# Optimization experiments

Hardware: AMD Instinct MI355X
Metric: run time of the kernel (lower is better)

The kernel has to match this reference:

```python
import jax, jax.numpy as jnp
import numpy as np

LATENT_DIM = 512
ASSET_DIM = 8192


def setup_inputs() -> dict:
    key = jax.random.key(0)
    ks = jax.random.split(key, 7)
    d = LATENT_DIM
    s = 1.0 / np.sqrt(d)  # torch Linear default init scale (uniform bound)
    z = jax.random.normal(ks[0], (ASSET_DIM, d), dtype=jnp.float32)
    Wq = jax.random.uniform(ks[1], (d, d), jnp.float32, -s, s)
    Wk = jax.random.uniform(ks[2], (d, d), jnp.float32, -s, s)
    Wv = jax.random.uniform(ks[3], (d, d), jnp.float32, -s, s)
    bq = jax.random.uniform(ks[4], (d,), jnp.float32, -s, s)
    bk = jax.random.uniform(ks[5], (d,), jnp.float32, -s, s)
    bv = jax.random.uniform(ks[6], (d,), jnp.float32, -s, s)
    return {"z": z, "Wq": Wq, "bq": bq, "Wk": Wk, "bk": bk, "Wv": Wv, "bv": bv}


def reference(z, Wq, bq, Wk, bk, Wv, bv):
    # z: (N, D). Single-head self-attention over assets.
    d = z.shape[-1]
    scale = d ** (-0.5)
    q = z @ Wq.T + bq          # (N, D)
    k = z @ Wk.T + bk          # (N, D)
    v = z @ Wv.T + bv          # (N, D)
    scores = jnp.einsum('nd,md->nm', q, k) * scale   # (N, N)
    attn = jax.nn.softmax(scores, axis=-1)
    # Original does attn[:, :, None] * v[None] then sum(dim=1); identical math:
    h = attn @ v               # (N, D)
    return h
```

## Files before the change

kernel.cpp:

```cpp
#include <hip/hip_runtime.h>
#include <hip/hip_bf16.h>
#include <stdint.h>

#define D 512
#define N 8192

typedef __attribute__((ext_vector_type(8))) short short8;
typedef __attribute__((ext_vector_type(4))) float f32x4;

static __device__ __forceinline__ unsigned short f2bf(float f) {
  unsigned int u = __builtin_bit_cast(unsigned int, f);
  u += 0x7fffu + ((u >> 16) & 1u);
  return (unsigned short)(u >> 16);
}
static __device__ __forceinline__ float bf2f(unsigned short s) {
  unsigned int u = ((unsigned int)s) << 16;
  return __builtin_bit_cast(float, u);
}

typedef const __attribute__((address_space(1))) unsigned int* gas_ptr;
typedef __attribute__((address_space(3))) unsigned int* las_ptr;
static __device__ __forceinline__ void gload_lds16(const void* g, void* l) {
  __builtin_amdgcn_global_load_lds((gas_ptr)g, (las_ptr)l, 16, 0, 0);
}

__global__ void cast_z_k(const float* __restrict__ z, unsigned short* __restrict__ zb) {
  int i = blockIdx.x * 256 + threadIdx.x;
  const int n4 = N * D / 4;
  for (; i < n4; i += gridDim.x * 256) {
    float4 v = ((const float4*)z)[i];
    ushort4 o = { f2bf(v.x), f2bf(v.y), f2bf(v.z), f2bf(v.w) };
    ((ushort4*)zb)[i] = o;
  }
}

__global__ void cast_w_k(const float* __restrict__ Wq, const float* __restrict__ Wk,
                         const float* __restrict__ Wv, const float* __restrict__ bq,
                         const float* __restrict__ bk, const float* __restrict__ bv,
                         unsigned short* __restrict__ wb, float* __restrict__ bqkv) {
  const float scale = 0.044194173824159216f;
  int i = blockIdx.x * 256 + threadIdx.x;
  const int per = D * D / 4;
  if (i < 3 * per) {
    int sec = i / per;
    int w4 = i - sec * per;
    const float* W = sec == 0 ? Wq : (sec == 1 ? Wk : Wv);
    float s = sec == 0 ? scale : 1.0f;
    float4 v = ((const float4*)W)[w4];
    ushort4 o = { f2bf(v.x * s), f2bf(v.y * s), f2bf(v.z * s), f2bf(v.w * s) };
    ((ushort4*)wb)[sec * per + w4] = o;
  }
  if (i < 3 * D) {
    int sec = i >> 9, j = i & (D - 1);
    const float* b = sec == 0 ? bq : (sec == 1 ? bk : bv);
    bqkv[i] = b[j] * (sec == 0 ? scale : 1.0f);
  }
}

#define BM 128
#define BN 128
#define BK 64

template <int EPI>
__global__ __launch_bounds__(256) void gemm_nt(
    const unsigned short* __restrict__ A, int lda,
    const unsigned short* __restrict__ B, int ldb,
    int K, int tiles_n,
    const float* __restrict__ bias,
    unsigned short* __restrict__ o0, unsigned short* __restrict__ o1,
    unsigned short* __restrict__ o2) {
  __shared__ unsigned short Ash[2][BM * BK];
  __shared__ unsigned short Bsh[2][BN * BK];

  const int t = threadIdx.x;
  const int w = t >> 6, lane = t & 63;
  const int bid = blockIdx.x, nwg = gridDim.x;
  const int cpx = nwg >> 3;
  const int swz = (bid & 7) * cpx + (bid >> 3);
  int tm, tn, kt0 = 0, nkt = K / BK, sidx = 0;
  if constexpr (EPI == 3) {
    sidx = swz >> 8;
    const int tile = swz & 255;
    tm = tile >> 2;
    tn = tile & 3;
    kt0 = sidx * 43;
    nkt = (sidx < 2) ? 43 : 42;
  } else {
    tm = swz / tiles_n;
    tn = swz - tm * tiles_n;
  }
  const int row0 = tm * BM, col0 = tn * BN;

  const int srow = t >> 3;
  const int scol = ((t & 7) ^ ((t >> 3) & 7)) * 8;
  const unsigned short* Ab = A + (size_t)(row0 + srow) * lda + scol;
  const unsigned short* Bb = B + (size_t)(col0 + srow) * ldb + scol;
  const int ldsbase = (w * 64) * 8;

  const int l15 = lane & 15, lhi = lane >> 4, lx = lane & 7;
  const int wr = w >> 1, wc = w & 1;
  const int arow = (wr * 64 + l15) * BK;
  const int brow = (wc * 64 + l15) * BK;
  const int ko0 = ((0 + lhi) ^ lx) * 8;
  const int ko1 = ((4 + lhi) ^ lx) * 8;

  f32x4 acc[4][4] = {};

  auto stage = [&](int buf, int k0) {
    const unsigned short* a = Ab + k0;
    const unsigned short* b = Bb + k0;
    unsigned short* la = &Ash[buf][ldsbase];
    unsigned short* lb = &Bsh[buf][ldsbase];
#pragma unroll
    for (int i = 0; i < 4; ++i) {
      gload_lds16(a + (size_t)(i * 32) * lda, la + i * 2048);
      gload_lds16(b + (size_t)(i * 32) * ldb, lb + i * 2048);
    }
  };

  stage(0, kt0 * BK);
  asm volatile("s_waitcnt vmcnt(0)" ::: "memory");
  __syncthreads();
  int cur = 0;
  for (int kt = 0; kt < nkt; ++kt) {
    if (kt + 1 < nkt) stage(cur ^ 1, (kt0 + kt + 1) * BK);
    const unsigned short* As = Ash[cur];
    const unsigned short* Bs = Bsh[cur];
#pragma unroll
    for (int ks = 0; ks < 2; ++ks) {
      const int ko = ks ? ko1 : ko0;
      short8 af[4], bg[4];
#pragma unroll
      for (int rf = 0; rf < 4; ++rf)
        af[rf] = *(const short8*)(As + arow + rf * (16 * BK) + ko);
#pragma unroll
      for (int cf = 0; cf < 4; ++cf)
        bg[cf] = *(const short8*)(Bs + brow + cf * (16 * BK) + ko);
#pragma unroll
      for (int rf = 0; rf < 4; ++rf)
#pragma unroll
        for (int cf = 0; cf < 4; ++cf)
          acc[rf][cf] = __builtin_amdgcn_mfma_f32_16x16x32_bf16(af[rf], bg[cf], acc[rf][cf], 0, 0, 0);
    }
    asm volatile("s_waitcnt vmcnt(0)" ::: "memory");
    __syncthreads();
    cur ^= 1;
  }

  const int r0g = row0 + wr * 64;
  const int c0g = col0 + wc * 64;

  if constexpr (EPI == 0) {
    const int sec = col0 >> 9;
#pragma unroll
    for (int cf = 0; cf < 4; ++cf) {
      const int c = c0g + cf * 16 + l15;
      const int cj = c & (D - 1);
      const float bb = bias[c];
#pragma unroll
      for (int rf = 0; rf < 4; ++rf) {
        const int r = r0g + rf * 16 + lhi * 4;
        f32x4 v = acc[rf][cf];
        if (sec == 0) {
#pragma unroll
          for (int g = 0; g < 4; ++g) o0[(size_t)(r + g) * D + cj] = f2bf(v[g] + bb);
        } else if (sec == 1) {
#pragma unroll
          for (int g = 0; g < 4; ++g) o1[(size_t)(r + g) * D + cj] = f2bf(v[g] + bb);
        } else {
          ushort4 o = { f2bf(v[0] + bb), f2bf(v[1] + bb), f2bf(v[2] + bb), f2bf(v[3] + bb) };
          *(ushort4*)(o2 + (size_t)cj * N + r) = o;
        }
      }
    }
  }

  if constexpr (EPI == 3) {
    unsigned short* op = o0 + (size_t)sidx * ((size_t)N * D);
#pragma unroll
    for (int cf = 0; cf < 4; ++cf) {
      const int c = c0g + cf * 16 + l15;
#pragma unroll
      for (int rf = 0; rf < 4; ++rf) {
        const int r = r0g + rf * 16 + lhi * 4;
        f32x4 v = acc[rf][cf];
#pragma unroll
        for (int g = 0; g < 4; ++g) op[(size_t)(r + g) * D + c] = f2bf(v[g]);
      }
    }
  }
}

__global__ __launch_bounds__(512, 2) void qk_exp_8ph(
    const unsigned short* __restrict__ A,
    const unsigned short* __restrict__ B,
    unsigned short* __restrict__ P,
    float* __restrict__ lpart) {
  __shared__ unsigned short Ash[2][256 * 64];
  __shared__ unsigned short Bsh[2][256 * 64];

  const int t = threadIdx.x;
  const int w = t >> 6, lane = t & 63;
  const int bid = blockIdx.x;
  const int swz = (bid & 7) * 128 + (bid >> 3);
  const int tm = swz >> 5, tn = swz & 31;
  const int row0 = tm * 256, col0 = tn * 256;

  const int wr = w >> 2, wc = w & 3;
  const int l15 = lane & 15, lhi = lane >> 4, lx = lane & 7;

  const int sr = t >> 3;
  const int ss = ((t & 7) ^ (sr & 7)) * 8;
  const unsigned short* Ab = A + (size_t)(row0 + sr) * D + ss;
  const unsigned short* Bb = B + (size_t)(col0 + sr) * D + ss;
  const int ldst = t * 8;

  const int aRowB = (wr * 128 + l15) * 64;
  const int bRowB = (wc * 64 + l15) * 64;
  const int sl0 = ((0 + lhi) ^ lx) * 8;
  const int sl1 = ((4 + lhi) ^ lx) * 8;

  f32x4 acc[8][4] = {};
  short8 af[4][2], bf[2][2];

#define STAGE8(buf, kt)                                                     \
  do {                                                                      \
    const unsigned short* a_ = Ab + (kt) * 64;                              \
    const unsigned short* b_ = Bb + (kt) * 64;                              \
    unsigned short* la_ = &Ash[buf][0];                                     \
    unsigned short* lb_ = &Bsh[buf][0];                                     \
    gload_lds16(a_, la_ + ldst);                                            \
    gload_lds16(a_ + (size_t)64 * D, la_ + 4096 + ldst);                    \
    gload_lds16(a_ + (size_t)128 * D, la_ + 8192 + ldst);                   \
    gload_lds16(a_ + (size_t)192 * D, la_ + 12288 + ldst);                  \
    gload_lds16(b_, lb_ + ldst);                                            \
    gload_lds16(b_ + (size_t)64 * D, lb_ + 4096 + ldst);                    \
    gload_lds16(b_ + (size_t)128 * D, lb_ + 8192 + ldst);                   \
    gload_lds16(b_ + (size_t)192 * D, lb_ + 12288 + ldst);                  \
  } while (0)

#define RDA(kk, mh)                                                          \
  do {                                                                       \
    _Pragma("unroll") for (int fm = 0; fm < 4; ++fm) {                       \
      const unsigned short* p_ = &Ash[kk][aRowB + (mh) * 4096 + fm * 1024];  \
      af[fm][0] = *(const short8*)(p_ + sl0);                                \
      af[fm][1] = *(const short8*)(p_ + sl1);                                \
    }                                                                        \
  } while (0)

#define RDB(kk, nh)                                                          \
  do {                                                                       \
    _Pragma("unroll") for (int fn = 0; fn < 2; ++fn) {                       \
      const unsigned short* p_ = &Bsh[kk][bRowB + (nh) * 2048 + fn * 1024];  \
      bf[fn][0] = *(const short8*)(p_ + sl0);                                \
      bf[fn][1] = *(const short8*)(p_ + sl1);                                \
    }                                                                        \
  } while (0)

#define MMA(mh, nh)                                                          \
  do {                                                                       \
    __builtin_amdgcn_s_setprio(1);                                           \
    _Pragma("unroll") for (int ks = 0; ks < 2; ++ks)                         \
      _Pragma("unroll") for (int fm = 0; fm < 4; ++fm)                       \
        _Pragma("unroll") for (int fn = 0; fn < 2; ++fn)                     \
          acc[(mh) * 4 + fm][(nh) * 2 + fn] =                                \
              __builtin_amdgcn_mfma_f32_16x16x32_bf16(                       \
                  af[fm][ks], bf[fn][ks], acc[(mh) * 4 + fm][(nh) * 2 + fn], \
                  0, 0, 0);                                                  \
    __builtin_amdgcn_s_setprio(0);                                           \
  } while (0)

#define BARLG()                                         \
  do {                                                  \
    __builtin_amdgcn_s_barrier();                       \
    asm volatile("s_waitcnt lgkmcnt(0)" ::: "memory");  \
    __builtin_amdgcn_sched_barrier(0);                  \
  } while (0)

#define VMDRAIN() asm volatile("s_waitcnt vmcnt(0)" ::: "memory")
#define POSTBAR() __builtin_amdgcn_s_barrier()

  STAGE8(0, 0);
  VMDRAIN();
  __builtin_amdgcn_s_barrier();

  const int NI = (D / 64) / 2;
  for (int i = 0; i < NI; ++i) {
    RDA(0, 0); RDB(0, 0);
    STAGE8(1, 2 * i + 1);
    BARLG(); MMA(0, 0); POSTBAR();

    RDB(0, 1);
    BARLG(); MMA(0, 1); POSTBAR();

    RDA(0, 1);
    BARLG(); MMA(1, 1); POSTBAR();

    RDB(0, 0);
    VMDRAIN();
    BARLG(); MMA(1, 0); POSTBAR();

    RDA(1, 0); RDB(1, 0);
    if (i + 1 < NI) STAGE8(0, 2 * i + 2);
    BARLG(); MMA(0, 0); POSTBAR();

    RDB(1, 1);
    BARLG(); MMA(0, 1); POSTBAR();

    RDA(1, 1);
    BARLG(); MMA(1, 1); POSTBAR();

    RDB(1, 0);
    if (i + 1 < NI) VMDRAIN();
    BARLG(); MMA(1, 0); POSTBAR();
  }

#pragma unroll
  for (int fm = 0; fm < 8; ++fm) {
    const int r = row0 + wr * 128 + fm * 16 + lhi * 4;
    float rs[4] = {0.f, 0.f, 0.f, 0.f};
#pragma unroll
    for (int fn = 0; fn < 4; ++fn) {
      const int c = col0 + wc * 64 + fn * 16 + l15;
      f32x4 v = acc[fm][fn];
#pragma unroll
      for (int g = 0; g < 4; ++g) {
        unsigned short us = f2bf(__expf(v[g]));
        P[(size_t)(r + g) * N + c] = us;
        rs[g] += bf2f(us);
      }
    }
#pragma unroll
    for (int g = 0; g < 4; ++g) {
      float s = rs[g];
      s += __shfl_xor(s, 1);
      s += __shfl_xor(s, 2);
      s += __shfl_xor(s, 4);
      s += __shfl_xor(s, 8);
      if (l15 == 0) lpart[(size_t)(tn * 4 + wc) * N + r + g] = s;
    }
  }
#undef STAGE8
#undef RDA
#undef RDB
#undef MMA
#undef BARLG
#undef VMDRAIN
#undef POSTBAR
}

__global__ void linv_k(const float* __restrict__ lpart, float* __restrict__ linv) {
  const int m = blockIdx.x * 256 + threadIdx.x;
  float s = 0.f;
  for (int i = 0; i < 128; ++i) s += lpart[(size_t)i * N + m];
  linv[m] = 1.0f / s;
}

__global__ void reduce_k(const unsigned short* __restrict__ Opart,
                         const float* __restrict__ linv, float* __restrict__ out) {
  const int i = blockIdx.x * 256 + threadIdx.x;
  const int m = i >> 7;
  const float li = linv[m];
  const size_t nd = (size_t)N * D;
  ushort4 a = ((const ushort4*)Opart)[i];
  ushort4 b = ((const ushort4*)(Opart + nd))[i];
  ushort4 c = ((const ushort4*)(Opart + 2 * nd))[i];
  float4 o;
  o.x = (bf2f(a.x) + bf2f(b.x) + bf2f(c.x)) * li;
  o.y = (bf2f(a.y) + bf2f(b.y) + bf2f(c.y)) * li;
  o.z = (bf2f(a.z) + bf2f(b.z) + bf2f(c.z)) * li;
  o.w = (bf2f(a.w) + bf2f(b.w) + bf2f(c.w)) * li;
  ((float4*)out)[i] = o;
}

extern "C" void kernel_launch(void* const* d_in, const int* in_sizes, int n_in,
                              void* d_out, int out_size, void* d_ws, size_t ws_size,
                              hipStream_t stream) {
  const float* z  = (const float*)d_in[0];
  const float* Wq = (const float*)d_in[1];
  const float* bq = (const float*)d_in[2];
  const float* Wk = (const float*)d_in[3];
  const float* bk = (const float*)d_in[4];
  const float* Wv = (const float*)d_in[5];
  const float* bv = (const float*)d_in[6];
  float* out = (float*)d_out;

  char* ws = (char*)d_ws;
  unsigned short* zb = (unsigned short*)(ws + 0);
  unsigned short* qb = (unsigned short*)(ws + 8388608);
  unsigned short* kb = (unsigned short*)(ws + 16777216);
  unsigned short* vT = (unsigned short*)(ws + 25165824);
  unsigned short* wb = (unsigned short*)(ws + 33554432);
  float* linv       = (float*)(ws + 33554432);
  float* bqkv       = (float*)(ws + 35127296);
  float* lpart      = (float*)(ws + 35133440);
  unsigned short* P = (unsigned short*)(ws + 39327744);
  unsigned short* Opart = (unsigned short*)(ws + 0);

  cast_z_k<<<dim3(2048), dim3(256), 0, stream>>>(z, zb);
  cast_w_k<<<dim3(768), dim3(256), 0, stream>>>(Wq, Wk, Wv, bq, bk, bv, wb, bqkv);

  gemm_nt<0><<<dim3(64 * 12), dim3(256), 0, stream>>>(
      zb, D, wb, D, D, 12, bqkv, qb, kb, vT);

  qk_exp_8ph<<<dim3(1024), dim3(512), 0, stream>>>(qb, kb, P, lpart);

  linv_k<<<dim3(32), dim3(256), 0, stream>>>(lpart, linv);

  gemm_nt<3><<<dim3(768), dim3(256), 0, stream>>>(
      P, N, vT, N, N, 4, (const float*)nullptr, Opart, (unsigned short*)nullptr,
      (unsigned short*)nullptr);

  reduce_k<<<dim3(4096), dim3(256), 0, stream>>>(Opart, linv, out);
}
```

Measured before the change: 254.1 us.

## Use 256x256 eight-phase pipelined kernel for PV GEMM with 4-way split-K

Result: faster. 227.2 us (median of 2 runs) (-10.6%).

```diff
diff --git a/kernel.cpp b/kernel.cpp
--- a/kernel.cpp
+++ b/kernel.cpp
@@ -57,50 +57,32 @@
   }
 }
 
-#define BM 128
-#define BN 128
-#define BK 64
-
-template <int EPI>
-__global__ __launch_bounds__(256) void gemm_nt(
-    const unsigned short* __restrict__ A, int lda,
-    const unsigned short* __restrict__ B, int ldb,
-    int K, int tiles_n,
+__global__ __launch_bounds__(256) void proj_qkv(
+    const unsigned short* __restrict__ A,
+    const unsigned short* __restrict__ B,
     const float* __restrict__ bias,
     unsigned short* __restrict__ o0, unsigned short* __restrict__ o1,
     unsigned short* __restrict__ o2) {
-  __shared__ unsigned short Ash[2][BM * BK];
-  __shared__ unsigned short Bsh[2][BN * BK];
+  __shared__ unsigned short Ash[2][128 * 64];
+  __shared__ unsigned short Bsh[2][128 * 64];
 
   const int t = threadIdx.x;
   const int w = t >> 6, lane = t & 63;
-  const int bid = blockIdx.x, nwg = gridDim.x;
-  const int cpx = nwg >> 3;
-  const int swz = (bid & 7) * cpx + (bid >> 3);
-  int tm, tn, kt0 = 0, nkt = K / BK, sidx = 0;
-  if constexpr (EPI == 3) {
-    sidx = swz >> 8;
-    const int tile = swz & 255;
-    tm = tile >> 2;
-    tn = tile & 3;
-    kt0 = sidx * 43;
-    nkt = (sidx < 2) ? 43 : 42;
-  } else {
-    tm = swz / tiles_n;
-    tn = swz - tm * tiles_n;
-  }
-  const int row0 = tm * BM, col0 = tn * BN;
+  const int bid = blockIdx.x;
+  const int swz = (bid & 7) * 96 + (bid >> 3);
+  const int tm = swz / 12, tn = swz - tm * 12;
+  const int row0 = tm * 128, col0 = tn * 128;
 
   const int srow = t >> 3;
   const int scol = ((t & 7) ^ ((t >> 3) & 7)) * 8;
-  const unsigned short* Ab = A + (size_t)(row0 + srow) * lda + scol;
-  const unsigned short* Bb = B + (size_t)(col0 + srow) * ldb + scol;
+  const unsigned short* Ab = A + (size_t)(row0 + srow) * D + scol;
+  const unsigned short* Bb = B + (size_t)(col0 + srow) * D + scol;
   const int ldsbase = (w * 64) * 8;
 
   const int l15 = lane & 15, lhi = lane >> 4, lx = lane & 7;
   const int wr = w >> 1, wc = w & 1;
-  const int arow = (wr * 64 + l15) * BK;
-  const int brow = (wc * 64 + l15) * BK;
+  const int arow = (wr * 64 + l15) * 64;
+  const int brow = (wc * 64 + l15) * 64;
   const int ko0 = ((0 + lhi) ^ lx) * 8;
   const int ko1 = ((4 + lhi) ^ lx) * 8;
 
@@ -113,17 +95,17 @@
     unsigned short* lb = &Bsh[buf][ldsbase];
 #pragma unroll
     for (int i = 0; i < 4; ++i) {
-      gload_lds16(a + (size_t)(i * 32) * lda, la + i * 2048);
-      gload_lds16(b + (size_t)(i * 32) * ldb, lb + i * 2048);
+      gload_lds16(a + (size_t)(i * 32) * D, la + i * 2048);
+      gload_lds16(b + (size_t)(i * 32) * D, lb + i * 2048);
     }
   };
 
-  stage(0, kt0 * BK);
+  stage(0, 0);
   asm volatile("s_waitcnt vmcnt(0)" ::: "memory");
   __syncthreads();
   int cur = 0;
-  for (int kt = 0; kt < nkt; ++kt) {
-    if (kt + 1 < nkt) stage(cur ^ 1, (kt0 + kt + 1) * BK);
+  for (int kt = 0; kt < 8; ++kt) {
+    if (kt + 1 < 8) stage(cur ^ 1, (kt + 1) * 64);
     const unsigned short* As = Ash[cur];
     const unsigned short* Bs = Bsh[cur];
 #pragma unroll
@@ -132,10 +114,10 @@
       short8 af[4], bg[4];
 #pragma unroll
       for (int rf = 0; rf < 4; ++rf)
-        af[rf] = *(const short8*)(As + arow + rf * (16 * BK) + ko);
+        af[rf] = *(const short8*)(As + arow + rf * (16 * 64) + ko);
 #pragma unroll
       for (int cf = 0; cf < 4; ++cf)
-        bg[cf] = *(const short8*)(Bs + brow + cf * (16 * BK) + ko);
+        bg[cf] = *(const short8*)(Bs + brow + cf * (16 * 64) + ko);
 #pragma unroll
       for (int rf = 0; rf < 4; ++rf)
 #pragma unroll
@@ -149,94 +131,44 @@
 
   const int r0g = row0 + wr * 64;
   const int c0g = col0 + wc * 64;
-
-  if constexpr (EPI == 0) {
-    const int sec = col0 >> 9;
-#pragma unroll
-    for (int cf = 0; cf < 4; ++cf) {
-      const int c = c0g + cf * 16 + l15;
-      const int cj = c & (D - 1);
-      const float bb = bias[c];
-#pragma unroll
-      for (int rf = 0; rf < 4; ++rf) {
-        const int r = r0g + rf * 16 + lhi * 4;
-        f32x4 v = acc[rf][cf];
-        if (sec == 0) {
-#pragma unroll
-          for (int g = 0; g < 4; ++g) o0[(size_t)(r + g) * D + cj] = f2bf(v[g] + bb);
-        } else if (sec == 1) {
-#pragma unroll
-          for (int g = 0; g < 4; ++g) o1[(size_t)(r + g) * D + cj] = f2bf(v[g] + bb);
-        } else {
-          ushort4 o = { f2bf(v[0] + bb), f2bf(v[1] + bb), f2bf(v[2] + bb), f2bf(v[3] + bb) };
-          *(ushort4*)(o2 + (size_t)cj * N + r) = o;
-        }
+  const int sec = col0 >> 9;
+#pragma unroll
+  for (int cf = 0; cf < 4; ++cf) {
+    const int c = c0g + cf * 16 + l15;
+    const int cj = c & (D - 1);
+    const float bb = bias[c];
+#pragma unroll
+    for (int rf = 0; rf < 4; ++rf) {
+      const int r = r0g + rf * 16 + lhi * 4;
+      f32x4 v = acc[rf][cf];
+      if (sec == 0) {
+#pragma unroll
+        for (int g = 0; g < 4; ++g) o0[(size_t)(r + g) * D + cj] = f2bf(v[g] + bb);
+      } else if (sec == 1) {
+#pragma unroll
+        for (int g = 0; g < 4; ++g) o1[(size_t)(r + g) * D + cj] = f2bf(v[g] + bb);
+      } else {
+        ushort4 o = { f2bf(v[0] + bb), f2bf(v[1] + bb), f2bf(v[2] + bb), f2bf(v[3] + bb) };
+        *(ushort4*)(o2 + (size_t)cj * N + r) = o;
       }
     }
   }
-
-  if constexpr (EPI == 3) {
-    unsigned short* op = o0 + (size_t)sidx * ((size_t)N * D);
-#pragma unroll
-    for (int cf = 0; cf < 4; ++cf) {
-      const int c = c0g + cf * 16 + l15;
-#pragma unroll
-      for (int rf = 0; rf < 4; ++rf) {
-        const int r = r0g + rf * 16 + lhi * 4;
-        f32x4 v = acc[rf][cf];
-#pragma unroll
-        for (int g = 0; g < 4; ++g) op[(size_t)(r + g) * D + c] = f2bf(v[g]);
-      }
-    }
-  }
-}
-
-__global__ __launch_bounds__(512, 2) void qk_exp_8ph(
-    const unsigned short* __restrict__ A,
-    const unsigned short* __restrict__ B,
-    unsigned short* __restrict__ P,
-    float* __restrict__ lpart) {
-  __shared__ unsigned short Ash[2][256 * 64];
-  __shared__ unsigned short Bsh[2][256 * 64];
-
-  const int t = threadIdx.x;
-  const int w = t >> 6, lane = t & 63;
-  const int bid = blockIdx.x;
-  const int swz = (bid & 7) * 128 + (bid >> 3);
-  const int tm = swz >> 5, tn = swz & 31;
-  const int row0 = tm * 256, col0 = tn * 256;
-
-  const int wr = w >> 2, wc = w & 3;
-  const int l15 = lane & 15, lhi = lane >> 4, lx = lane & 7;
-
-  const int sr = t >> 3;
-  const int ss = ((t & 7) ^ (sr & 7)) * 8;
-  const unsigned short* Ab = A + (size_t)(row0 + sr) * D + ss;
-  const unsigned short* Bb = B + (size_t)(col0 + sr) * D + ss;
-  const int ldst = t * 8;
-
-  const int aRowB = (wr * 128 + l15) * 64;
-  const int bRowB = (wc * 64 + l15) * 64;
-  const int sl0 = ((0 + lhi) ^ lx) * 8;
-  const int sl1 = ((4 + lhi) ^ lx) * 8;
-
-  f32x4 acc[8][4] = {};
-  short8 af[4][2], bf[2][2];
-
-#define STAGE8(buf, kt)                                                     \
+}
+
+#define STAGE8(buf, kt, LDB)                                                \
   do {                                                                      \
-    const unsigned short* a_ = Ab + (kt) * 64;                              \
-    const unsigned short* b_ = Bb + (kt) * 64;                              \
+    const unsigned short* a_ = Ab + (size_t)(kt) * 64;                      \
+    const unsigned short* b_ = Bb + (size_t)(kt) * 64;                      \
     unsigned short* la_ = &Ash[buf][0];                                     \
     unsigned short* lb_ = &Bsh[buf][0];                                     \
     gload_lds16(a_, la_ + ldst);                                            \
-    gload_lds16(a_ + (size_t)64 * D, la_ + 4096 + ldst);                    \
-    gload_lds16(a_ + (size_t)128 * D, la_ + 8192 + ldst);                   \
-    gload_lds16(a_ + (size_t)192 * D, la_ + 12288 + ldst);                  \
+    gload_lds16(a_ + (size_t)64 * (LDB), la_ + 4096 + ldst);                \
+    gload_lds16(a_ + (size_t)128 * (LDB), la_ + 8192 + ldst);               \
+    gload_lds16(a_ + (size_t)192 * (LDB), la_ + 12288 + ldst);              \
     gload_lds16(b_, lb_ + ldst);                                            \
-    gload_lds16(b_ + (size_t)64 * D, lb_ + 4096 + ldst);                    \
-    gload_lds16(b_ + (size_t)128 * D, lb_ + 8192 + ldst);                   \
-    gload_lds16(b_ + (size_t)192 * D, lb_ + 12288 + ldst);                  \
+    gload_lds16(b_ + (size_t)64 * (LDB), lb_ + 4096 + ldst);                \
+    gload_lds16(b_ + (size_t)128 * (LDB), lb_ + 8192 + ldst);               \
+    gload_lds16(b_ + (size_t)192 * (LDB), lb_ + 12288 + ldst);              \
   } while (0)
 
 #define RDA(kk, mh)                                                          \
@@ -280,40 +212,66 @@
 #define VMDRAIN() asm volatile("s_waitcnt vmcnt(0)" ::: "memory")
 #define POSTBAR() __builtin_amdgcn_s_barrier()
 
-  STAGE8(0, 0);
-  VMDRAIN();
-  __builtin_amdgcn_s_barrier();
-
-  const int NI = (D / 64) / 2;
-  for (int i = 0; i < NI; ++i) {
-    RDA(0, 0); RDB(0, 0);
-    STAGE8(1, 2 * i + 1);
-    BARLG(); MMA(0, 0); POSTBAR();
-
-    RDB(0, 1);
-    BARLG(); MMA(0, 1); POSTBAR();
-
-    RDA(0, 1);
-    BARLG(); MMA(1, 1); POSTBAR();
-
-    RDB(0, 0);
-    VMDRAIN();
-    BARLG(); MMA(1, 0); POSTBAR();
-
-    RDA(1, 0); RDB(1, 0);
-    if (i + 1 < NI) STAGE8(0, 2 * i + 2);
-    BARLG(); MMA(0, 0); POSTBAR();
-
-    RDB(1, 1);
-    BARLG(); MMA(0, 1); POSTBAR();
-
-    RDA(1, 1);
-    BARLG(); MMA(1, 1); POSTBAR();
-
-    RDB(1, 0);
-    if (i + 1 < NI) VMDRAIN();
-    BARLG(); MMA(1, 0); POSTBAR();
-  }
+#define EIGHT_PHASE_LOOP(NI, KT0, LDB)                              \
+  STAGE8(0, (KT0), LDB);                                            \
+  VMDRAIN();                                                        \
+  __builtin_amdgcn_s_barrier();                                     \
+  for (int i = 0; i < (NI); ++i) {                                  \
+    RDA(0, 0); RDB(0, 0);                                           \
+    STAGE8(1, (KT0) + 2 * i + 1, LDB);                              \
+    BARLG(); MMA(0, 0); POSTBAR();                                  \
+    RDB(0, 1);                                                      \
+    BARLG(); MMA(0, 1); POSTBAR();                                  \
+    RDA(0, 1);                                                      \
+    BARLG(); MMA(1, 1); POSTBAR();                                  \
+    RDB(0, 0);                                                      \
+    VMDRAIN();                                                      \
+    BARLG(); MMA(1, 0); POSTBAR();                                  \
+    RDA(1, 0); RDB(1, 0);                                           \
+    if (i + 1 < (NI)) STAGE8(0, (KT0) + 2 * i + 2, LDB);            \
+    BARLG(); MMA(0, 0); POSTBAR();                                  \
+    RDB(1, 1);                                                      \
+    BARLG(); MMA(0, 1); POSTBAR();                                  \
+    RDA(1, 1);                                                      \
+    BARLG(); MMA(1, 1); POSTBAR();                                  \
+    RDB(1, 0);                                                      \
+    if (i + 1 < (NI)) VMDRAIN();                                    \
+    BARLG(); MMA(1, 0); POSTBAR();                                  \
+  }
+
+__global__ __launch_bounds__(512, 2) void qk_exp_8ph(
+    const unsigned short* __restrict__ A,
+    const unsigned short* __restrict__ B,
+    unsigned short* __restrict__ P,
+    float* __restrict__ lpart) {
+  __shared__ unsigned short Ash[2][256 * 64];
+  __shared__ unsigned short Bsh[2][256 * 64];
+
+  const int t = threadIdx.x;
+  const int w = t >> 6, lane = t & 63;
+  const int bid = blockIdx.x;
+  const int swz = (bid & 7) * 128 + (bid >> 3);
+  const int tm = swz >> 5, tn = swz & 31;
+  const int row0 = tm * 256, col0 = tn * 256;
+
+  const int wr = w >> 2, wc = w & 3;
+  const int l15 = lane & 15, lhi = lane >> 4, lx = lane & 7;
+
+  const int sr = t >> 3;
+  const int ss = ((t & 7) ^ (sr & 7)) * 8;
+  const unsigned short* Ab = A + (size_t)(row0 + sr) * D + ss;
+  const unsigned short* Bb = B + (size_t)(col0 + sr) * D + ss;
+  const int ldst = t * 8;
+
+  const int aRowB = (wr * 128 + l15) * 64;
+  const int bRowB = (wc * 64 + l15) * 64;
+  const int sl0 = ((0 + lhi) ^ lx) * 8;
+  const int sl1 = ((4 + lhi) ^ lx) * 8;
+
+  f32x4 acc[8][4] = {};
+  short8 af[4][2], bf[2][2];
+
+  EIGHT_PHASE_LOOP(4, 0, D)
 
 #pragma unroll
   for (int fm = 0; fm < 8; ++fm) {
@@ -340,13 +298,71 @@
       if (l15 == 0) lpart[(size_t)(tn * 4 + wc) * N + r + g] = s;
     }
   }
-#undef STAGE8
-#undef RDA
-#undef RDB
-#undef MMA
-#undef BARLG
-#undef VMDRAIN
-#undef POSTBAR
+}
+
+__global__ __launch_bounds__(512, 2) void pv_8ph(
+    const unsigned short* __restrict__ A,
+    const unsigned short* __restrict__ B,
+    unsigned short* __restrict__ Opart,
+    float* __restrict__ outF) {
+  __shared__ unsigned short Ash[2][256 * 64];
+  __shared__ unsigned short Bsh[2][256 * 64];
+
+  const int t = threadIdx.x;
+  const int w = t >> 6, lane = t & 63;
+  const int bid = blockIdx.x;
+  const int swz = (bid & 7) * 32 + (bid >> 3);
+  const int sp = swz >> 6;
+  const int idx = swz & 63;
+  const int tm = idx >> 1, tn = idx & 1;
+  const int row0 = tm * 256, col0 = tn * 256;
+  const int kt0 = sp * 32;
+
+  const int wr = w >> 2, wc = w & 3;
+  const int l15 = lane & 15, lhi = lane >> 4, lx = lane & 7;
+
+  const int sr = t >> 3;
+  const int ss = ((t & 7) ^ (sr & 7)) * 8;
+  const unsigned short* Ab = A + (size_t)(row0 + sr) * N + ss;
+  const unsigned short* Bb = B + (size_t)(col0 + sr) * N + ss;
+  const int ldst = t * 8;
+
+  const int aRowB = (wr * 128 + l15) * 64;
+  const int bRowB = (wc * 64 + l15) * 64;
+  const int sl0 = ((0 + lhi) ^ lx) * 8;
+  const int sl1 = ((4 + lhi) ^ lx) * 8;
+
+  f32x4 acc[8][4] = {};
+  short8 af[4][2], bf[2][2];
+
+  EIGHT_PHASE_LOOP(16, kt0, N)
+
+  if (sp < 3) {
+    unsigned short* op = Opart + (size_t)sp * ((size_t)N * D);
+#pragma unroll
+    for (int fm = 0; fm < 8; ++fm) {
+      const int r = row0 + wr * 128 + fm * 16 + lhi * 4;
+#pragma unroll
+      for (int fn = 0; fn < 4; ++fn) {
+        const int c = col0 + wc * 64 + fn * 16 + l15;
+        f32x4 v = acc[fm][fn];
+#pragma unroll
+        for (int g = 0; g < 4; ++g) op[(size_t)(r + g) * D + c] = f2bf(v[g]);
+      }
+    }
+  } else {
+#pragma unroll
+    for (int fm = 0; fm < 8; ++fm) {
+      const int r = row0 + wr * 128 + fm * 16 + lhi * 4;
+#pragma unroll
+      for (int fn = 0; fn < 4; ++fn) {
+        const int c = col0 + wc * 64 + fn * 16 + l15;
+        f32x4 v = acc[fm][fn];
+#pragma unroll
+        for (int g = 0; g < 4; ++g) outF[(size_t)(r + g) * D + c] = v[g];
+      }
+    }
+  }
 }
 
 __global__ void linv_k(const float* __restrict__ lpart, float* __restrict__ linv) {
@@ -365,11 +381,11 @@
   ushort4 a = ((const ushort4*)Opart)[i];
   ushort4 b = ((const ushort4*)(Opart + nd))[i];
   ushort4 c = ((const ushort4*)(Opart + 2 * nd))[i];
-  float4 o;
-  o.x = (bf2f(a.x) + bf2f(b.x) + bf2f(c.x)) * li;
-  o.y = (bf2f(a.y) + bf2f(b.y) + bf2f(c.y)) * li;
-  o.z = (bf2f(a.z) + bf2f(b.z) + bf2f(c.z)) * li;
-  o.w = (bf2f(a.w) + bf2f(b.w) + bf2f(c.w)) * li;
+  float4 o = ((float4*)out)[i];
+  o.x = (bf2f(a.x) + bf2f(b.x) + bf2f(c.x) + o.x) * li;
+  o.y = (bf2f(a.y) + bf2f(b.y) + bf2f(c.y) + o.y) * li;
+  o.z = (bf2f(a.z) + bf2f(b.z) + bf2f(c.z) + o.z) * li;
+  o.w = (bf2f(a.w) + bf2f(b.w) + bf2f(c.w) + o.w) * li;
   ((float4*)out)[i] = o;
 }
 
@@ -400,16 +416,13 @@
   cast_z_k<<<dim3(2048), dim3(256), 0, stream>>>(z, zb);
   cast_w_k<<<dim3(768), dim3(256), 0, stream>>>(Wq, Wk, Wv, bq, bk, bv, wb, bqkv);
 
-  gemm_nt<0><<<dim3(64 * 12), dim3(256), 0, stream>>>(
-      zb, D, wb, D, D, 12, bqkv, qb, kb, vT);
+  proj_qkv<<<dim3(768), dim3(256), 0, stream>>>(zb, wb, bqkv, qb, kb, vT);
 
   qk_exp_8ph<<<dim3(1024), dim3(512), 0, stream>>>(qb, kb, P, lpart);
 
   linv_k<<<dim3(32), dim3(256), 0, stream>>>(lpart, linv);
 
-  gemm_nt<3><<<dim3(768), dim3(256), 0, stream>>>(
-      P, N, vT, N, N, 4, (const float*)nullptr, Opart, (unsigned short*)nullptr,
-      (unsigned short*)nullptr);
+  pv_8ph<<<dim3(256), dim3(512), 0, stream>>>(P, vT, Opart, out);
 
   reduce_k<<<dim3(4096), dim3(256), 0, stream>>>(Opart, linv, out);
 }
```
